# Kernel tuning notes

Measured on AMD Instinct MI355X. Metric: run time of the kernel, lower is better.

The kernel has to match this reference:

```python
import jax, jax.numpy as jnp
import numpy as np

N = 100000      # nodes
E = 1600000     # edges (avg degree 16)
D_IN, D_H, D_OUT = 128, 128, 64


def setup_inputs() -> dict:
    key = jax.random.key(0)
    k1, k2, k3, k4 = jax.random.split(key, 4)
    x = jax.random.normal(k1, (N, D_IN), dtype=jnp.float32)
    edge_index = jax.random.randint(k2, (2, E), 0, N, dtype=jnp.int32)
    W1 = jax.random.normal(k3, (D_IN, D_H), dtype=jnp.float32) * (1.0 / np.sqrt(D_IN))
    b1 = jnp.zeros((D_H,), dtype=jnp.float32)
    W2 = jax.random.normal(k4, (D_H, D_OUT), dtype=jnp.float32) * (1.0 / np.sqrt(D_H))
    b2 = jnp.zeros((D_OUT,), dtype=jnp.float32)
    return {"x": x, "edge_index": edge_index, "W1": W1, "b1": b1, "W2": W2, "b2": b2}


def _gcn_conv(x, src, dst, W, b):
    """PyG GCNConv: out = D^{-1/2} (A + I) D^{-1/2} (x W) + b."""
    n = x.shape[0]
    h = x @ W  # [N, D_out] — transform first, then aggregate (PyG order)
    loops = jnp.arange(n, dtype=src.dtype)
    src_f = jnp.concatenate([src, loops])
    dst_f = jnp.concatenate([dst, loops])
    deg = jax.ops.segment_sum(jnp.ones_like(dst_f, dtype=h.dtype), dst_f, num_segments=n)
    dinv = jax.lax.rsqrt(deg)  # deg >= 1 due to self-loops
    norm = dinv[src_f] * dinv[dst_f]            # [E+N]
    msg = h[src_f] * norm[:, None]              # [E+N, D_out] gather
    out = jax.ops.segment_sum(msg, dst_f, num_segments=n)  # scatter-add
    return out + b


def reference(x, edge_index, W1, b1, W2, b2):
    src, dst = edge_index[0], edge_index[1]
    h = jax.nn.relu(_gcn_conv(x, src, dst, W1, b1))
    o = _gcn_conv(h, src, dst, W2, b2)
    return jax.nn.log_softmax(o, axis=1)
```

## Files before the change

### kernel.cpp

```cpp
#include <hip/hip_runtime.h>
#include <hip/hip_bf16.h>

typedef __hip_bfloat16 bf16;
typedef short short8 __attribute__((ext_vector_type(8)));
typedef float f32x4 __attribute__((ext_vector_type(4)));
typedef float f32x2 __attribute__((ext_vector_type(2)));

#define NPB 256
#define MAXBUK 1024

__device__ __forceinline__ float bf2f_raw(unsigned short u) {
    unsigned x = ((unsigned)u) << 16; float f; __builtin_memcpy(&f, &x, 4); return f;
}
__device__ __forceinline__ unsigned short f2bf_raw(float f) {
    unsigned u; __builtin_memcpy(&u, &f, 4);
    u += 0x7FFFu + ((u >> 16) & 1u);
    return (unsigned short)(u >> 16);
}
__device__ __forceinline__ float lo_f(unsigned u) {
    unsigned x = u << 16; float f; __builtin_memcpy(&f, &x, 4); return f;
}
__device__ __forceinline__ float hi_f(unsigned u) {
    unsigned x = u & 0xffff0000u; float f; __builtin_memcpy(&f, &x, 4); return f;
}


__global__ __launch_bounds__(256) void fatA_kernel(const unsigned short* __restrict__ W1s,
                                                   const void* __restrict__ W1p,
                                                   const void* __restrict__ W2p,
                                                   const void* __restrict__ b1p,
                                                   const void* __restrict__ b2p,
                                                   unsigned short* __restrict__ WB1,
                                                   unsigned short* __restrict__ WB2,
                                                   float* __restrict__ b1f,
                                                   float* __restrict__ b2f,
                                                   int* __restrict__ flag, int nshorts,
                                                   const int* __restrict__ dst,
                                                   int* __restrict__ bktcnt,
                                                   int E, int nbuk, int prepb) {
    __shared__ int smem[MAXBUK];
    const int tt = threadIdx.x;
    if ((int)blockIdx.x < prepb) {
        const int sample = min(nshorts, 2048);
        int c = 0;
        for (int i = tt; i < sample; i += 256) {
            unsigned e = (W1s[i] >> 7) & 0xFFu;
            if (e >= 140u || (e >= 1u && e <= 40u)) c++;
        }
        smem[tt] = c;
        __syncthreads();
        for (int o = 128; o > 0; o >>= 1) {
            if (tt < o) smem[tt] += smem[tt + o];
            __syncthreads();
        }
        const int isf32 = (smem[0] > sample / 8) ? 1 : 0;
        if (blockIdx.x == 0 && tt == 0) *flag = isf32;

        const int t = blockIdx.x * 256 + tt;
        const int T1 = 16384, T2 = 8192;
        if (t < T1) {
            int j = t & 7, l = (t >> 3) & 63, f = t >> 9;
            int n = f >> 2, kk = f & 3;
            int k = kk * 32 + (l >> 4) * 8 + j;
            int col = n * 16 + (l & 15);
            WB1[t] = isf32 ? f2bf_raw(((const float*)W1p)[k * 128 + col])
                           : ((const unsigned short*)W1p)[k * 128 + col];
        } else if (t < T1 + T2) {
            int o = t - T1;
            int j = o & 7, l = (o >> 3) & 63, f = o >> 9;
            int n = f >> 2, kk = f & 3;
            int k = kk * 32 + (l >> 4) * 8 + j;
            int col = n * 16 + (l & 15);
            WB2[o] = isf32 ? f2bf_raw(((const float*)W2p)[k * 64 + col])
                           : ((const unsigned short*)W2p)[k * 64 + col];
        } else if (t < T1 + T2 + 128) {
            int o = t - T1 - T2;
            b1f[o] = isf32 ? ((const float*)b1p)[o] : bf2f_raw(((const unsigned short*)b1p)[o]);
        } else if (t < T1 + T2 + 192) {
            int o = t - T1 - T2 - 128;
            b2f[o] = isf32 ? ((const float*)b2p)[o] : bf2f_raw(((const unsigned short*)b2p)[o]);
        }
    } else {
        const int e0 = ((int)blockIdx.x - prepb) * 4096;
        const int e1 = min(E, e0 + 4096);
        for (int b = tt; b < nbuk; b += 256) smem[b] = 0;
        __syncthreads();
        for (int e = e0 + tt; e < e1; e += 256) atomicAdd(&smem[dst[e] >> 8], 1);
        __syncthreads();
        for (int b = tt; b < nbuk; b += 256) {
            int c = smem[b];
            if (c) atomicAdd(&bktcnt[b], c);
        }
    }
}

__global__ __launch_bounds__(1024) void bscan_kernel(const int* __restrict__ bktcnt,
                                                     int* __restrict__ bofs,
                                                     int* __restrict__ bcur,
                                                     int nbuk, int total) {
    __shared__ int ps[1024];
    const int t = threadIdx.x;
    int v = (t < nbuk) ? bktcnt[t] : 0;
    ps[t] = v;
    __syncthreads();
    for (int o = 1; o < 1024; o <<= 1) {
        int u = (t >= o) ? ps[t - o] : 0;
        __syncthreads();
        ps[t] += u;
        __syncthreads();
    }
    if (t < nbuk) {
        int ex = ps[t] - v;
        bofs[t] = ex;
        bcur[t] = ex;
    }
    if (t == 0) bofs[nbuk] = total;
}


__global__ __launch_bounds__(256) void fatB_kernel(const void* __restrict__ Xp,
                                                   const unsigned short* __restrict__ WB1,
                                                   unsigned char* __restrict__ Hf8, int nrows,
                                                   const int* __restrict__ flag,
                                                   const int* __restrict__ src,
                                                   const int* __restrict__ dst,
                                                   int* __restrict__ bcur,
                                                   unsigned* __restrict__ packed,
                                                   int E, int nbuk, int gb) {
    __shared__ __align__(16) char smem[52224];
    const int t = threadIdx.x;
    if ((int)blockIdx.x < gb) {
        unsigned short* Xs = (unsigned short*)smem;
        unsigned short* Cs = (unsigned short*)(smem + 34816);
        const int r0 = blockIdx.x * 128;
        const int isf32 = *flag;

        if (isf32) {
            const float4* Xg = (const float4*)Xp;
            #pragma unroll
            for (int i = 0; i < 16; ++i) {
                int idx = t + 256 * i;
                int row = idx >> 5, c4 = idx & 31;
                float4 v = {0.f, 0.f, 0.f, 0.f};
                if (r0 + row < nrows) v = Xg[(size_t)(r0 + row) * 32 + c4];
                unsigned lo = (unsigned)f2bf_raw(v.x) | ((unsigned)f2bf_raw(v.y) << 16);
                unsigned hi = (unsigned)f2bf_raw(v.z) | ((unsigned)f2bf_raw(v.w) << 16);
                *reinterpret_cast<uint2*>(&Xs[row * 136 + c4 * 4]) = make_uint2(lo, hi);
            }
        } else {
            const uint4* Xg = (const uint4*)Xp;
            #pragma unroll
            for (int i = 0; i < 8; ++i) {
                int idx = t + 256 * i;
                int row = idx >> 4, c8 = idx & 15;
                uint4 v = {0u, 0u, 0u, 0u};
                if (r0 + row < nrows) v = Xg[(size_t)(r0 + row) * 16 + c8];
                *reinterpret_cast<uint4*>(&Xs[row * 136 + c8 * 8]) = v;
            }
        }
        __syncthreads();

        const int lane = t & 63, w = t >> 6;
        const int m0 = w * 32;
        short8 a[2][4];
        #pragma unroll
        for (int rt = 0; rt < 2; ++rt)
            #pragma unroll
            for (int kk = 0; kk < 4; ++kk)
                a[rt][kk] = *reinterpret_cast<const short8*>(
                    &Xs[(m0 + rt * 16 + (lane & 15)) * 136 + kk * 32 + (lane >> 4) * 8]);

        for (int p = 0; p < 2; ++p) {
            short8 b[4][4];
            #pragma unroll
            for (int n = 0; n < 4; ++n)
                #pragma unroll
                for (int kk = 0; kk < 4; ++kk)
                    b[n][kk] = *reinterpret_cast<const short8*>(
                        WB1 + (size_t)(((p * 4 + n) * 4 + kk) * 64 + lane) * 8);
            f32x4 acc[2][4];
            #pragma unroll
            for (int rt = 0; rt < 2; ++rt)
                #pragma unroll
                for (int n = 0; n < 4; ++n) {
                    acc[rt][n] = (f32x4){0.f, 0.f, 0.f, 0.f};
                    #pragma unroll
                    for (int kk = 0; kk < 4; ++kk)
                        acc[rt][n] = __builtin_amdgcn_mfma_f32_16x16x32_bf16(
                            a[rt][kk], b[n][kk], acc[rt][n], 0, 0, 0);
                }
            if (p) __syncthreads();
            #pragma unroll
            for (int rt = 0; rt < 2; ++rt)
                #pragma unroll
                for (int n = 0; n < 4; ++n)
                    #pragma unroll
                    for (int r = 0; r < 4; ++r) {
                        int row = m0 + rt * 16 + (lane >> 4) * 4 + r;
                        Cs[row * 68 + n * 16 + (lane & 15)] = f2bf_raw(acc[rt][n][r]);
                    }
            __syncthreads();
            #pragma unroll
            for (int i = 0; i < 4; ++i) {
                int idx = t + 256 * i;
                int row = idx >> 3, c8 = idx & 7;
                if (r0 + row < nrows) {
                    uint2 va = *reinterpret_cast<const uint2*>(&Cs[row * 68 + c8 * 8]);
                    uint2 vb = *reinterpret_cast<const uint2*>(&Cs[row * 68 + c8 * 8 + 4]);
                    int w0 = __builtin_amdgcn_cvt_pk_fp8_f32(lo_f(va.x), hi_f(va.x), 0, false);
                    w0 = __builtin_amdgcn_cvt_pk_fp8_f32(lo_f(va.y), hi_f(va.y), w0, true);
                    int w1 = __builtin_amdgcn_cvt_pk_fp8_f32(lo_f(vb.x), hi_f(vb.x), 0, false);
                    w1 = __builtin_amdgcn_cvt_pk_fp8_f32(lo_f(vb.y), hi_f(vb.y), w1, true);
                    *reinterpret_cast<uint2*>(Hf8 + (size_t)(r0 + row) * 128 + p * 64 + c8 * 8) =
                        make_uint2((unsigned)w0, (unsigned)w1);
                }
            }
            if (!p) __syncthreads();
        }
    } else {
        int* cnt = (int*)smem;
        int* gbase = (int*)(smem + 4096);
        const int e0 = ((int)blockIdx.x - gb) * 4096;
        const int e1 = min(E, e0 + 4096);
        for (int b = t; b < nbuk; b += 256) cnt[b] = 0;
        __syncthreads();
        for (int e = e0 + t; e < e1; e += 256) atomicAdd(&cnt[dst[e] >> 8], 1);
        __syncthreads();
        for (int b = t; b < nbuk; b += 256) {
            int c = cnt[b];
            gbase[b] = c ? atomicAdd(&bcur[b], c) : 0;
            cnt[b] = 0;
        }
        __syncthreads();
        for (int e = e0 + t; e < e1; e += 256) {
            int d = dst[e];
            int b = d >> 8;
            int r = atomicAdd(&cnt[b], 1);
            packed[gbase[b] + r] = ((unsigned)(d & 255) << 24) | (unsigned)src[e];
        }
    }
}

__global__ __launch_bounds__(256) void csr_fine2_kernel(const unsigned* __restrict__ packed,
                                                        const int* __restrict__ bofs,
                                                        uint2* __restrict__ nmeta,
                                                        float* __restrict__ dinv,
                                                        unsigned* __restrict__ epu, int n) {
    __shared__ int cnt2[NPB];
    __shared__ int cur[NPB];
    const int t = threadIdx.x;
    const int b = blockIdx.x;
    const int node0 = b << 8;
    const int nn = min(NPB, n - node0);
    cnt2[t] = 0;
    __syncthreads();
    const int beg = bofs[b], end = bofs[b + 1];
    for (int i = beg + t; i < end; i += 256) atomicAdd(&cnt2[packed[i] >> 24], 1);
    __syncthreads();
    int c = cnt2[t];
    cur[t] = c;
    __syncthreads();
    for (int o = 1; o < 256; o <<= 1) {
        int u = (t >= o) ? cur[t - o] : 0;
        __syncthreads();
        cur[t] += u;
        __syncthreads();
    }
    const int base = beg + cur[t] - c;
    if (t < nn) {
        nmeta[node0 + t] = make_uint2((unsigned)base, (unsigned)c);
        dinv[node0 + t] = rsqrtf((float)(c + 1));
    }
    __syncthreads();
    cur[t] = base;
    __syncthreads();
    for (int i = beg + t; i < end; i += 256) {
        unsigned u = packed[i];
        int pos = atomicAdd(&cur[u >> 24], 1);
        epu[2 * pos] = u & 0xFFFFFFu;
    }
}

__global__ __launch_bounds__(256) void epw_kernel(unsigned* __restrict__ epu,
                                                  const float* __restrict__ dinv, int E) {
    int i = blockIdx.x * 256 + threadIdx.x;
    if (i < E) {
        unsigned s = epu[2 * i];
        float w = dinv[s];
        unsigned wb; __builtin_memcpy(&wb, &w, 4);
        epu[2 * i + 1] = wb;
    }
}


__device__ __forceinline__ float epw_f(uint2 e) {
    float w; __builtin_memcpy(&w, &e.y, 4); return w;
}

__device__ __forceinline__ void accf8_2(f32x2* acc, uint2 v, float w) {
    f32x2 wv = {w, w};
    acc[0] += __builtin_amdgcn_cvt_pk_f32_fp8(v.x, false) * wv;
    acc[1] += __builtin_amdgcn_cvt_pk_f32_fp8(v.x, true)  * wv;
    acc[2] += __builtin_amdgcn_cvt_pk_f32_fp8(v.y, false) * wv;
    acc[3] += __builtin_amdgcn_cvt_pk_f32_fp8(v.y, true)  * wv;
}

__global__ __launch_bounds__(128) void agg128_v9(const uint2* __restrict__ H2,
                                                 const uint2* __restrict__ nmeta,
                                                 const uint2* __restrict__ epack,
                                                 const float* __restrict__ biasf,
                                                 uint4* __restrict__ G4, int n) {
    const int lane = threadIdx.x & 63;
    const int g = lane >> 4;
    const int sub = lane & 15;
    const int node = blockIdx.x * 2 + (threadIdx.x >> 6);
    if (node >= n) return;

    uint2 vself = H2[((unsigned)node << 4) + (unsigned)sub];

    const uint2 meta = nmeta[node];
    const int base = (int)meta.x;
    const int cnt = (int)meta.y;
    const int end = base + cnt;
    const float di = rsqrtf((float)(cnt + 1));

    f32x2 acc[4];
    #pragma unroll
    for (int i = 0; i < 4; ++i) acc[i] = (f32x2){0.f, 0.f};
    accf8_2(acc, vself, (g == 0) ? di : 0.f);

    int j = base;
    for (; j + 15 < end; j += 16) {
        uint2 e0 = epack[j + g];
        uint2 e1 = epack[j + 4 + g];
        uint2 e2 = epack[j + 8 + g];
        uint2 e3 = epack[j + 12 + g];
        uint2 v0 = H2[(e0.x << 4) + (unsigned)sub];
        uint2 v1 = H2[(e1.x << 4) + (unsigned)sub];
        uint2 v2 = H2[(e2.x << 4) + (unsigned)sub];
        uint2 v3 = H2[(e3.x << 4) + (unsigned)sub];
        accf8_2(acc, v0, epw_f(e0));
        accf8_2(acc, v1, epw_f(e1));
        accf8_2(acc, v2, epw_f(e2));
        accf8_2(acc, v3, epw_f(e3));
    }
    for (; j + 7 < end; j += 8) {
        uint2 e0 = epack[j + g];
        uint2 e1 = epack[j + 4 + g];
        uint2 v0 = H2[(e0.x << 4) + (unsigned)sub];
        uint2 v1 = H2[(e1.x << 4) + (unsigned)sub];
        accf8_2(acc, v0, epw_f(e0));
        accf8_2(acc, v1, epw_f(e1));
    }
    for (; j + 3 < end; j += 4) {
        uint2 e0 = epack[j + g];
        uint2 v0 = H2[(e0.x << 4) + (unsigned)sub];
        accf8_2(acc, v0, epw_f(e0));
    }
    if (j + g < end) {
        uint2 e0 = epack[j + g];
        uint2 v0 = H2[(e0.x << 4) + (unsigned)sub];
        accf8_2(acc, v0, epw_f(e0));
    }

    float a8[8];
    #pragma unroll
    for (int i = 0; i < 4; ++i) { a8[2 * i] = acc[i].x; a8[2 * i + 1] = acc[i].y; }
    #pragma unroll
    for (int i = 0; i < 8; ++i) {
        a8[i] += __shfl_xor(a8[i], 16, 64);
        a8[i] += __shfl_xor(a8[i], 32, 64);
    }

    if (g == 0) {
        const float4* b4 = (const float4*)biasf;
        float4 blo = b4[sub * 2], bhi = b4[sub * 2 + 1];
        a8[0] = fmaxf(fmaf(di, a8[0], blo.x), 0.f);
        a8[1] = fmaxf(fmaf(di, a8[1], blo.y), 0.f);
        a8[2] = fmaxf(fmaf(di, a8[2], blo.z), 0.f);
        a8[3] = fmaxf(fmaf(di, a8[3], blo.w), 0.f);
        a8[4] = fmaxf(fmaf(di, a8[4], bhi.x), 0.f);
        a8[5] = fmaxf(fmaf(di, a8[5], bhi.y), 0.f);
        a8[6] = fmaxf(fmaf(di, a8[6], bhi.z), 0.f);
        a8[7] = fmaxf(fmaf(di, a8[7], bhi.w), 0.f);
        uint4 o;
        o.x = (unsigned)f2bf_raw(a8[0]) | ((unsigned)f2bf_raw(a8[1]) << 16);
        o.y = (unsigned)f2bf_raw(a8[2]) | ((unsigned)f2bf_raw(a8[3]) << 16);
        o.z = (unsigned)f2bf_raw(a8[4]) | ((unsigned)f2bf_raw(a8[5]) << 16);
        o.w = (unsigned)f2bf_raw(a8[6]) | ((unsigned)f2bf_raw(a8[7]) << 16);
        G4[((unsigned)node << 4) + (unsigned)sub] = o;
    }
}


__global__ __launch_bounds__(256) void gemm2b_mfma(const unsigned short* __restrict__ X,
                                                   const unsigned short* __restrict__ WB2,
                                                   unsigned short* __restrict__ T, int nrows) {
    __shared__ __align__(16) unsigned short Xs[128 * 136];
    __shared__ __align__(16) unsigned short Cs[128 * 68];
    const int t = threadIdx.x;
    const int r0 = blockIdx.x * 128;

    const uint4* Xg = (const uint4*)X;
    #pragma unroll
    for (int i = 0; i < 8; ++i) {
        int idx = t + 256 * i;
        int row = idx >> 4, c8 = idx & 15;
        uint4 v = {0u, 0u, 0u, 0u};
        if (r0 + row < nrows) v = Xg[(size_t)(r0 + row) * 16 + c8];
        *reinterpret_cast<uint4*>(&Xs[row * 136 + c8 * 8]) = v;
    }
    __syncthreads();

    const int lane = t & 63, w = t >> 6;
    const int m0 = w * 32;
    short8 a[2][4];
    #pragma unroll
    for (int rt = 0; rt < 2; ++rt)
        #pragma unroll
        for (int kk = 0; kk < 4; ++kk)
            a[rt][kk] = *reinterpret_cast<const short8*>(
                &Xs[(m0 + rt * 16 + (lane & 15)) * 136 + kk * 32 + (lane >> 4) * 8]);

    short8 b[4][4];
    #pragma unroll
    for (int n = 0; n < 4; ++n)
        #pragma unroll
        for (int kk = 0; kk < 4; ++kk)
            b[n][kk] = *reinterpret_cast<const short8*>(
                WB2 + (size_t)((n * 4 + kk) * 64 + lane) * 8);

    f32x4 acc[2][4];
    #pragma unroll
    for (int rt = 0; rt < 2; ++rt)
        #pragma unroll
        for (int n = 0; n < 4; ++n) {
            acc[rt][n] = (f32x4){0.f, 0.f, 0.f, 0.f};
            #pragma unroll
            for (int kk = 0; kk < 4; ++kk)
                acc[rt][n] = __builtin_amdgcn_mfma_f32_16x16x32_bf16(
                    a[rt][kk], b[n][kk], acc[rt][n], 0, 0, 0);
        }

    __syncthreads();
    #pragma unroll
    for (int rt = 0; rt < 2; ++rt)
        #pragma unroll
        for (int n = 0; n < 4; ++n)
            #pragma unroll
            for (int r = 0; r < 4; ++r) {
                int row = m0 + rt * 16 + (lane >> 4) * 4 + r;
                Cs[row * 68 + n * 16 + (lane & 15)] = f2bf_raw(acc[rt][n][r]);
            }
    __syncthreads();
    #pragma unroll
    for (int i = 0; i < 8; ++i) {
        int idx = t + 256 * i;
        int row = idx >> 4, c4 = idx & 15;
        if (r0 + row < nrows) {
            uint2 v = *reinterpret_cast<const uint2*>(&Cs[row * 68 + c4 * 4]);
            *reinterpret_cast<uint2*>(T + (size_t)(r0 + row) * 64 + c4 * 4) = v;
        }
    }
}


__device__ __forceinline__ void acc8v(f32x2* acc, uint4 v, float w) {
    f32x2 wv = {w, w};
    acc[0] += (f32x2){lo_f(v.x), hi_f(v.x)} * wv;
    acc[1] += (f32x2){lo_f(v.y), hi_f(v.y)} * wv;
    acc[2] += (f32x2){lo_f(v.z), hi_f(v.z)} * wv;
    acc[3] += (f32x2){lo_f(v.w), hi_f(v.w)} * wv;
}

__global__ __launch_bounds__(128) void agg64_final(const uint4* __restrict__ T4,
                                                   const uint2* __restrict__ nmeta,
                                                   const uint2* __restrict__ epack,
                                                   const float* __restrict__ b2f,
                                                   void* __restrict__ OUTv, int n,
                                                   const int* __restrict__ flag) {
    const int lane = threadIdx.x & 63;
    const int g = lane >> 3;
    const int sub = lane & 7;
    const int node = blockIdx.x * 2 + (threadIdx.x >> 6);
    if (node >= n) return;
    const int outf32 = *flag;

    const unsigned selfoff = ((unsigned)node << 3) + (unsigned)sub;
    uint4 vself = T4[selfoff];

    const uint2 meta = nmeta[node];
    const int base = (int)meta.x;
    const int cnt = (int)meta.y;
    const int end = base + cnt;
    const float di = rsqrtf((float)(cnt + 1));

    f32x2 acc[4];
    {
        const float ws = (g == 0) ? di : 0.f;
        acc[0] = (f32x2){ws * lo_f(vself.x), ws * hi_f(vself.x)};
        acc[1] = (f32x2){ws * lo_f(vself.y), ws * hi_f(vself.y)};
        acc[2] = (f32x2){ws * lo_f(vself.z), ws * hi_f(vself.z)};
        acc[3] = (f32x2){ws * lo_f(vself.w), ws * hi_f(vself.w)};
    }

    int j = base;
    for (; j + 15 < end; j += 16) {
        uint2 e0 = epack[j + g];
        uint2 e1 = epack[j + 8 + g];
        uint4 v0 = T4[(e0.x << 3) + (unsigned)sub];
        uint4 v1 = T4[(e1.x << 3) + (unsigned)sub];
        acc8v(acc, v0, epw_f(e0));
        acc8v(acc, v1, epw_f(e1));
    }
    for (; j + 7 < end; j += 8) {
        uint2 e0 = epack[j + g];
        uint4 v0 = T4[(e0.x << 3) + (unsigned)sub];
        acc8v(acc, v0, epw_f(e0));
    }
    if (j + g < end) {
        uint2 e0 = epack[j + g];
        uint4 v0 = T4[(e0.x << 3) + (unsigned)sub];
        acc8v(acc, v0, epw_f(e0));
    }

    float a8[8];
    #pragma unroll
    for (int i = 0; i < 4; ++i) { a8[2 * i] = acc[i].x; a8[2 * i + 1] = acc[i].y; }
    #pragma unroll
    for (int i = 0; i < 8; ++i) {
        a8[i] += __shfl_xor(a8[i], 8, 64);
        a8[i] += __shfl_xor(a8[i], 16, 64);
        a8[i] += __shfl_xor(a8[i], 32, 64);
    }

    if (g == 0) {
        const float4* b4 = (const float4*)b2f;
        float4 blo = b4[sub * 2], bhi = b4[sub * 2 + 1];
        a8[0] = fmaf(di, a8[0], blo.x);
        a8[1] = fmaf(di, a8[1], blo.y);
        a8[2] = fmaf(di, a8[2], blo.z);
        a8[3] = fmaf(di, a8[3], blo.w);
        a8[4] = fmaf(di, a8[4], bhi.x);
        a8[5] = fmaf(di, a8[5], bhi.y);
        a8[6] = fmaf(di, a8[6], bhi.z);
        a8[7] = fmaf(di, a8[7], bhi.w);

        float m = fmaxf(fmaxf(fmaxf(a8[0], a8[1]), fmaxf(a8[2], a8[3])),
                        fmaxf(fmaxf(a8[4], a8[5]), fmaxf(a8[6], a8[7])));
        m = fmaxf(m, __shfl_xor(m, 1, 64));
        m = fmaxf(m, __shfl_xor(m, 2, 64));
        m = fmaxf(m, __shfl_xor(m, 4, 64));
        float s = __expf(a8[0] - m) + __expf(a8[1] - m) + __expf(a8[2] - m) + __expf(a8[3] - m) +
                  __expf(a8[4] - m) + __expf(a8[5] - m) + __expf(a8[6] - m) + __expf(a8[7] - m);
        s += __shfl_xor(s, 1, 64);
        s += __shfl_xor(s, 2, 64);
        s += __shfl_xor(s, 4, 64);
        const float lse = m + __logf(s);

        if (outf32) {
            float4* Of = (float4*)OUTv;
            float4 o0 = {a8[0] - lse, a8[1] - lse, a8[2] - lse, a8[3] - lse};
            float4 o1 = {a8[4] - lse, a8[5] - lse, a8[6] - lse, a8[7] - lse};
            Of[(size_t)node * 16 + sub * 2] = o0;
            Of[(size_t)node * 16 + sub * 2 + 1] = o1;
        } else {
            uint4 o;
            o.x = (unsigned)f2bf_raw(a8[0] - lse) | ((unsigned)f2bf_raw(a8[1] - lse) << 16);
            o.y = (unsigned)f2bf_raw(a8[2] - lse) | ((unsigned)f2bf_raw(a8[3] - lse) << 16);
            o.z = (unsigned)f2bf_raw(a8[4] - lse) | ((unsigned)f2bf_raw(a8[5] - lse) << 16);
            o.w = (unsigned)f2bf_raw(a8[6] - lse) | ((unsigned)f2bf_raw(a8[7] - lse) << 16);
            ((uint4*)OUTv)[(size_t)node * 8 + sub] = o;
        }
    }
}


extern "C" void kernel_launch(void* const* d_in, const int* in_sizes, int n_in,
                              void* d_out, int out_size, void* d_ws, size_t ws_size,
                              hipStream_t stream) {
    const void* x  = d_in[0];
    const int*  ei = (const int*)d_in[1];
    const void* W1 = d_in[2];
    const void* b1 = d_in[3];
    const void* W2 = d_in[4];
    const void* b2 = d_in[5];

    const int N = in_sizes[0] / 128;
    const int E = in_sizes[1] / 2;
    const int* src = ei;
    const int* dst = ei + E;
    const int NBUK = (N + NPB - 1) / NPB;

    char* p = (char*)d_ws;
    auto alloc = [&](size_t bytes) { char* q = p; p += (bytes + 255) & ~255ull; return q; };
    int*   flag   = (int*)  alloc(4);
    uint2* nmeta  = (uint2*)alloc((size_t)N * 8);
    float* dinv   = (float*)alloc((size_t)N * 4);
    int*   bktcnt = (int*)  alloc((size_t)NBUK * 4);
    int*   bofs   = (int*)  alloc((size_t)(NBUK + 1) * 4);
    int*   bcur   = (int*)  alloc((size_t)NBUK * 4);
    float* b1f    = (float*)alloc(128 * 4);
    float* b2f    = (float*)alloc(64 * 4);
    unsigned short* WB1 = (unsigned short*)alloc(16384 * 2);
    unsigned short* WB2 = (unsigned short*)alloc(8192 * 2);
    unsigned* big = (unsigned*)alloc((size_t)N * 128 * 2);
    unsigned* packed = (unsigned*)d_out;
    uint2*    epack  = (uint2*)d_in[1];
    unsigned* g1 = (unsigned*)d_in[0];
    unsigned short* T = (unsigned short*)big;
    (void)ws_size; (void)n_in; (void)out_size;

    const int PREPB = 97;
    const int MSB = (E + 4095) / 4096;
    const int GB = (N + 127) / 128;

    hipMemsetAsync(bktcnt, 0, (size_t)NBUK * 4, stream);
    fatA_kernel<<<PREPB + MSB, 256, 0, stream>>>((const unsigned short*)W1, W1, W2, b1, b2,
                                                 WB1, WB2, b1f, b2f, flag, in_sizes[2],
                                                 dst, bktcnt, E, NBUK, PREPB);
    bscan_kernel<<<1, 1024, 0, stream>>>(bktcnt, bofs, bcur, NBUK, E);
    fatB_kernel<<<GB + MSB, 256, 0, stream>>>(x, WB1, (unsigned char*)big, N, flag,
                                              src, dst, bcur, packed, E, NBUK, GB);
    csr_fine2_kernel<<<NBUK, 256, 0, stream>>>(packed, bofs, nmeta, dinv, (unsigned*)epack, N);
    epw_kernel<<<(E + 255) / 256, 256, 0, stream>>>((unsigned*)epack, dinv, E);

    agg128_v9<<<(N + 1) / 2, 128, 0, stream>>>((const uint2*)big, nmeta, epack, b1f, (uint4*)g1, N);
    gemm2b_mfma<<<GB, 256, 0, stream>>>((const unsigned short*)g1, WB2, T, N);
    agg64_final<<<(N + 1) / 2, 128, 0, stream>>>((const uint4*)T, nmeta, epack, b2f, d_out, N, flag);
}
```

Measured before the change: 299.3 us.

## Alias LDS staging buffers and narrow agg64 lane mapping to 16 lanes/row

```diff
diff --git a/kernel.cpp b/kernel.cpp
--- a/kernel.cpp
+++ b/kernel.cpp
@@ -127,11 +127,11 @@
                                                    int* __restrict__ bcur,
                                                    unsigned* __restrict__ packed,
                                                    int E, int nbuk, int gb) {
-    __shared__ __align__(16) char smem[52224];
+    __shared__ __align__(16) char smem[34816];
     const int t = threadIdx.x;
     if ((int)blockIdx.x < gb) {
         unsigned short* Xs = (unsigned short*)smem;
-        unsigned short* Cs = (unsigned short*)(smem + 34816);
+        unsigned short* Cs = (unsigned short*)smem;
         const int r0 = blockIdx.x * 128;
         const int isf32 = *flag;
 
@@ -169,6 +169,7 @@
             for (int kk = 0; kk < 4; ++kk)
                 a[rt][kk] = *reinterpret_cast<const short8*>(
                     &Xs[(m0 + rt * 16 + (lane & 15)) * 136 + kk * 32 + (lane >> 4) * 8]);
+        __syncthreads();
 
         for (int p = 0; p < 2; ++p) {
             short8 b[4][4];
@@ -396,8 +397,9 @@
 __global__ __launch_bounds__(256) void gemm2b_mfma(const unsigned short* __restrict__ X,
                                                    const unsigned short* __restrict__ WB2,
                                                    unsigned short* __restrict__ T, int nrows) {
-    __shared__ __align__(16) unsigned short Xs[128 * 136];
-    __shared__ __align__(16) unsigned short Cs[128 * 68];
+    __shared__ __align__(16) char smem[34816];
+    unsigned short* Xs = (unsigned short*)smem;
+    unsigned short* Cs = (unsigned short*)smem;
     const int t = threadIdx.x;
     const int r0 = blockIdx.x * 128;
 
@@ -421,6 +423,7 @@
         for (int kk = 0; kk < 4; ++kk)
             a[rt][kk] = *reinterpret_cast<const short8*>(
                 &Xs[(m0 + rt * 16 + (lane & 15)) * 136 + kk * 32 + (lane >> 4) * 8]);
+    __syncthreads();
 
     short8 b[4][4];
     #pragma unroll
@@ -442,7 +445,6 @@
                     a[rt][kk], b[n][kk], acc[rt][n], 0, 0, 0);
         }
 
-    __syncthreads();
     #pragma unroll
     for (int rt = 0; rt < 2; ++rt)
         #pragma unroll
@@ -465,29 +467,26 @@
 }
 
 
-__device__ __forceinline__ void acc8v(f32x2* acc, uint4 v, float w) {
+__device__ __forceinline__ void acc4v(f32x2* acc, uint2 v, float w) {
     f32x2 wv = {w, w};
     acc[0] += (f32x2){lo_f(v.x), hi_f(v.x)} * wv;
     acc[1] += (f32x2){lo_f(v.y), hi_f(v.y)} * wv;
-    acc[2] += (f32x2){lo_f(v.z), hi_f(v.z)} * wv;
-    acc[3] += (f32x2){lo_f(v.w), hi_f(v.w)} * wv;
-}
-
-__global__ __launch_bounds__(128) void agg64_final(const uint4* __restrict__ T4,
+}
+
+__global__ __launch_bounds__(128) void agg64_final(const uint2* __restrict__ T2,
                                                    const uint2* __restrict__ nmeta,
                                                    const uint2* __restrict__ epack,
                                                    const float* __restrict__ b2f,
                                                    void* __restrict__ OUTv, int n,
                                                    const int* __restrict__ flag) {
     const int lane = threadIdx.x & 63;
-    const int g = lane >> 3;
-    const int sub = lane & 7;
+    const int g = lane >> 4;
+    const int sub = lane & 15;
     const int node = blockIdx.x * 2 + (threadIdx.x >> 6);
     if (node >= n) return;
     const int outf32 = *flag;
 
-    const unsigned selfoff = ((unsigned)node << 3) + (unsigned)sub;
-    uint4 vself = T4[selfoff];
+    uint2 vself = T2[((unsigned)node << 4) + (unsigned)sub];
 
     const uint2 meta = nmeta[node];
     const int base = (int)meta.x;
@@ -495,82 +494,82 @@
     const int end = base + cnt;
     const float di = rsqrtf((float)(cnt + 1));
 
-    f32x2 acc[4];
+    f32x2 acc[2];
     {
         const float ws = (g == 0) ? di : 0.f;
         acc[0] = (f32x2){ws * lo_f(vself.x), ws * hi_f(vself.x)};
         acc[1] = (f32x2){ws * lo_f(vself.y), ws * hi_f(vself.y)};
-        acc[2] = (f32x2){ws * lo_f(vself.z), ws * hi_f(vself.z)};
-        acc[3] = (f32x2){ws * lo_f(vself.w), ws * hi_f(vself.w)};
     }
 
     int j = base;
     for (; j + 15 < end; j += 16) {
         uint2 e0 = epack[j + g];
-        uint2 e1 = epack[j + 8 + g];
-        uint4 v0 = T4[(e0.x << 3) + (unsigned)sub];
-        uint4 v1 = T4[(e1.x << 3) + (unsigned)sub];
-        acc8v(acc, v0, epw_f(e0));
-        acc8v(acc, v1, epw_f(e1));
+        uint2 e1 = epack[j + 4 + g];
+        uint2 e2 = epack[j + 8 + g];
+        uint2 e3 = epack[j + 12 + g];
+        uint2 v0 = T2[(e0.x << 4) + (unsigned)sub];
+        uint2 v1 = T2[(e1.x << 4) + (unsigned)sub];
+        uint2 v2 = T2[(e2.x << 4) + (unsigned)sub];
+        uint2 v3 = T2[(e3.x << 4) + (unsigned)sub];
+        acc4v(acc, v0, epw_f(e0));
+        acc4v(acc, v1, epw_f(e1));
+        acc4v(acc, v2, epw_f(e2));
+        acc4v(acc, v3, epw_f(e3));
     }
     for (; j + 7 < end; j += 8) {
         uint2 e0 = epack[j + g];
-        uint4 v0 = T4[(e0.x << 3) + (unsigned)sub];
-        acc8v(acc, v0, epw_f(e0));
+        uint2 e1 = epack[j + 4 + g];
+        uint2 v0 = T2[(e0.x << 4) + (unsigned)sub];
+        uint2 v1 = T2[(e1.x << 4) + (unsigned)sub];
+        acc4v(acc, v0, epw_f(e0));
+        acc4v(acc, v1, epw_f(e1));
+    }
+    for (; j + 3 < end; j += 4) {
+        uint2 e0 = epack[j + g];
+        uint2 v0 = T2[(e0.x << 4) + (unsigned)sub];
+        acc4v(acc, v0, epw_f(e0));
     }
     if (j + g < end) {
         uint2 e0 = epack[j + g];
-        uint4 v0 = T4[(e0.x << 3) + (unsigned)sub];
-        acc8v(acc, v0, epw_f(e0));
-    }
-
-    float a8[8];
-    #pragma unroll
-    for (int i = 0; i < 4; ++i) { a8[2 * i] = acc[i].x; a8[2 * i + 1] = acc[i].y; }
-    #pragma unroll
-    for (int i = 0; i < 8; ++i) {
-        a8[i] += __shfl_xor(a8[i], 8, 64);
-        a8[i] += __shfl_xor(a8[i], 16, 64);
-        a8[i] += __shfl_xor(a8[i], 32, 64);
+        uint2 v0 = T2[(e0.x << 4) + (unsigned)sub];
+        acc4v(acc, v0, epw_f(e0));
+    }
+
+    float a4[4] = {acc[0].x, acc[0].y, acc[1].x, acc[1].y};
+    #pragma unroll
+    for (int i = 0; i < 4; ++i) {
+        a4[i] += __shfl_xor(a4[i], 16, 64);
+        a4[i] += __shfl_xor(a4[i], 32, 64);
     }
 
     if (g == 0) {
-        const float4* b4 = (const float4*)b2f;
-        float4 blo = b4[sub * 2], bhi = b4[sub * 2 + 1];
-        a8[0] = fmaf(di, a8[0], blo.x);
-        a8[1] = fmaf(di, a8[1], blo.y);
-        a8[2] = fmaf(di, a8[2], blo.z);
-        a8[3] = fmaf(di, a8[3], blo.w);
-        a8[4] = fmaf(di, a8[4], bhi.x);
-        a8[5] = fmaf(di, a8[5], bhi.y);
-        a8[6] = fmaf(di, a8[6], bhi.z);
-        a8[7] = fmaf(di, a8[7], bhi.w);
-
-        float m = fmaxf(fmaxf(fmaxf(a8[0], a8[1]), fmaxf(a8[2], a8[3])),
-                        fmaxf(fmaxf(a8[4], a8[5]), fmaxf(a8[6], a8[7])));
+        float4 bb = ((const float4*)b2f)[sub];
+        a4[0] = fmaf(di, a4[0], bb.x);
+        a4[1] = fmaf(di, a4[1], bb.y);
+        a4[2] = fmaf(di, a4[2], bb.z);
+        a4[3] = fmaf(di, a4[3], bb.w);
+
+        float m = fmaxf(fmaxf(a4[0], a4[1]), fmaxf(a4[2], a4[3]));
         m = fmaxf(m, __shfl_xor(m, 1, 64));
         m = fmaxf(m, __shfl_xor(m, 2, 64));
         m = fmaxf(m, __shfl_xor(m, 4, 64));
-        float s = __expf(a8[0] - m) + __expf(a8[1] - m) + __expf(a8[2] - m) + __expf(a8[3] - m) +
-                  __expf(a8[4] - m) + __expf(a8[5] - m) + __expf(a8[6] - m) + __expf(a8[7] - m);
+        m = fmaxf(m, __shfl_xor(m, 8, 64));
+        float s = __expf(a4[0] - m) + __expf(a4[1] - m) +
+                  __expf(a4[2] - m) + __expf(a4[3] - m);
         s += __shfl_xor(s, 1, 64);
         s += __shfl_xor(s, 2, 64);
         s += __shfl_xor(s, 4, 64);
+        s += __shfl_xor(s, 8, 64);
         const float lse = m + __logf(s);
 
         if (outf32) {
-            float4* Of = (float4*)OUTv;
-            float4 o0 = {a8[0] - lse, a8[1] - lse, a8[2] - lse, a8[3] - lse};
-            float4 o1 = {a8[4] - lse, a8[5] - lse, a8[6] - lse, a8[7] - lse};
-            Of[(size_t)node * 16 + sub * 2] = o0;
-            Of[(size_t)node * 16 + sub * 2 + 1] = o1;
+            float4 o = {a4[0] - lse, a4[1] - lse, a4[2] - lse, a4[3] - lse};
+            ((float4*)OUTv)[(size_t)node * 16 + sub] = o;
         } else {
-            uint4 o;
-            o.x = (unsigned)f2bf_raw(a8[0] - lse) | ((unsigned)f2bf_raw(a8[1] - lse) << 16);
-            o.y = (unsigned)f2bf_raw(a8[2] - lse) | ((unsigned)f2bf_raw(a8[3] - lse) << 16);
-            o.z = (unsigned)f2bf_raw(a8[4] - lse) | ((unsigned)f2bf_raw(a8[5] - lse) << 16);
-            o.w = (unsigned)f2bf_raw(a8[6] - lse) | ((unsigned)f2bf_raw(a8[7] - lse) << 16);
-            ((uint4*)OUTv)[(size_t)node * 8 + sub] = o;
+            uint2 o;
+            o.x = (unsigned)f2bf_raw(a4[0] - lse) | ((unsigned)f2bf_raw(a4[1] - lse) << 16);
+            o.y = (unsigned)f2bf_raw(a4[2] - lse) | ((unsigned)f2bf_raw(a4[3] - lse) << 16);
+            ((uint2*)OUTv)[(size_t)node * 16 + sub] = o;
         }
     }
 }
@@ -627,5 +626,5 @@
 
     agg128_v9<<<(N + 1) / 2, 128, 0, stream>>>((const uint2*)big, nmeta, epack, b1f, (uint4*)g1, N);
     gemm2b_mfma<<<GB, 256, 0, stream>>>((const unsigned short*)g1, WB2, T, N);
-    agg64_final<<<(N + 1) / 2, 128, 0, stream>>>((const uint4*)T, nmeta, epack, b2f, d_out, N, flag);
-}
+    agg64_final<<<(N + 1) / 2, 128, 0, stream>>>((const uint2*)T, nmeta, epack, b2f, d_out, N, flag);
+}
```

Result: no change. 294.0 us (-1.8%).
